# Performance work log

Measured on AMD Instinct MI355X. Metric: run time of the kernel, lower is better.

## Reference

```python
import jax, jax.numpy as jnp
import numpy as np

B, S, L = 4, 1024, 128
H, D = 16, 64            # num_attention_heads, attention_head_size
HID = H * D              # 1024
MAX_POS = 1024


def setup_inputs() -> dict:
    key = jax.random.key(0)
    ks = jax.random.split(key, 12)
    sc = 1.0 / np.sqrt(HID)
    return {
        "hidden_states": jax.random.normal(ks[0], (B, S, HID), jnp.float32),
        "attention_mask": jnp.zeros((B, 1, 1, S), jnp.float32),
        "instruct_hidden_states": jax.random.normal(ks[1], (B, L, HID), jnp.float32),
        "instruct_attention_mask": jnp.zeros((B, 1, 1, L), jnp.float32),
        "Wq": jax.random.normal(ks[2], (HID, HID), jnp.float32) * sc,
        "bq": jnp.zeros((HID,), jnp.float32),
        "Wk": jax.random.normal(ks[3], (HID, HID), jnp.float32) * sc,
        "bk": jnp.zeros((HID,), jnp.float32),
        "Wv": jax.random.normal(ks[4], (HID, HID), jnp.float32) * sc,
        "bv": jnp.zeros((HID,), jnp.float32),
        "gate": jnp.zeros((1, H, 1, 1), jnp.float32),
        "dist_emb": jax.random.normal(ks[5], (2 * MAX_POS - 1, D), jnp.float32) * 0.02,
    }


def _heads(x):
    # [B,T,HID] -> [B,H,T,D]
    b, t, _ = x.shape
    return x.reshape(b, t, H, D).transpose(0, 2, 1, 3)


def reference(hidden_states, attention_mask, instruct_hidden_states,
              instruct_attention_mask, Wq, bq, Wk, bk, Wv, bv, gate, dist_emb):
    inv_sqrt_d = 1.0 / jnp.sqrt(jnp.asarray(D, hidden_states.dtype))

    q = _heads(hidden_states @ Wq + bq)            # [B,H,S,D]
    k = _heads(hidden_states @ Wk + bk)
    v = _heads(hidden_states @ Wv + bv)
    ik = _heads(instruct_hidden_states @ Wk + bk)  # [B,H,L,D]
    iv = _heads(instruct_hidden_states @ Wv + bv)

    scores = jnp.einsum('bhld,bhrd->bhlr', q, k)   # [B,H,S,S]

    # relative_key_query positional scores
    pos = jnp.arange(S)
    dist_idx = pos[:, None] - pos[None, :] + MAX_POS - 1   # [S,S]
    pe = dist_emb[dist_idx]                                # [S,S,D]
    scores = scores + jnp.einsum('bhld,lrd->bhlr', q, pe) \
                    + jnp.einsum('bhrd,lrd->bhlr', k, pe)

    scores = scores * inv_sqrt_d + attention_mask
    probs = jax.nn.softmax(scores, axis=-1)
    ctx = jnp.einsum('bhlr,bhrd->bhld', probs, v)          # [B,H,S,D]

    # gated instruction attention
    iscores = jnp.einsum('bhld,bhrd->bhlr', q, ik) * inv_sqrt_d + instruct_attention_mask
    iprobs = jax.nn.softmax(iscores, axis=-1)
    ictx = jnp.einsum('bhlr,bhrd->bhld', iprobs, iv)
    ctx = ctx + jnp.tanh(gate) * ictx

    # [B,H,S,D] -> [B,S,HID]
    return ctx.transpose(0, 2, 1, 3).reshape(B, S, HID)
```

## Files before the change

kernel.cpp:

```cpp
#include <hip/hip_runtime.h>
#include <cmath>

#define NB 4
#define NH 16
#define SD 64
#define SEQ 1024
#define ILEN 128
#define HIDDIM 1024

#define N_HID (NB*SEQ*HIDDIM)
#define N_INS (NB*ILEN*HIDDIM)
#define N_E_SRC (2047*SD)
#define N_E   (2048*SD)
#define N_W   (HIDDIM*HIDDIM)

typedef short bf8 __attribute__((ext_vector_type(8)));
typedef short bf4 __attribute__((ext_vector_type(4)));
typedef float f4  __attribute__((ext_vector_type(4)));

#define MFMA(a,b,c) __builtin_amdgcn_mfma_f32_16x16x32_bf16(a,b,c,0,0,0)

#define SHIFT 12.0f

__device__ __forceinline__ float bf2f(short s) {
    unsigned u = ((unsigned)(unsigned short)s) << 16;
    return __uint_as_float(u);
}
__device__ __forceinline__ short f2bf(float x) {
    unsigned u = __float_as_uint(x);
    u = (u + 0x7FFFu + ((u >> 16) & 1u)) >> 16;
    return (short)u;
}

__global__ __launch_bounds__(256) void cast_flat(
    const float* __restrict__ hid, const float* __restrict__ ins,
    const float* __restrict__ E, short* __restrict__ ws)
{
    int i = (blockIdx.x * 256 + threadIdx.x) * 4;
    short* dhid = ws;
    short* dins = ws + N_HID;
    short* dE   = ws + N_HID + N_INS;
    if (i < N_HID) {
        float4 v = *(const float4*)&hid[i];
        bf4 o; o[0]=f2bf(v.x); o[1]=f2bf(v.y); o[2]=f2bf(v.z); o[3]=f2bf(v.w);
        *(bf4*)&dhid[i] = o;
    } else if (i < N_HID + N_INS) {
        int j = i - N_HID;
        float4 v = *(const float4*)&ins[j];
        bf4 o; o[0]=f2bf(v.x); o[1]=f2bf(v.y); o[2]=f2bf(v.z); o[3]=f2bf(v.w);
        *(bf4*)&dins[j] = o;
    } else {
        int j = i - N_HID - N_INS;
        if (j < N_E) {
            bf4 o;
            if (j < N_E_SRC) {
                float4 v = *(const float4*)&E[j];
                o[0]=f2bf(v.x); o[1]=f2bf(v.y); o[2]=f2bf(v.z); o[3]=f2bf(v.w);
            } else {
                o[0]=0; o[1]=0; o[2]=0; o[3]=0;
            }
            *(bf4*)&dE[j] = o;
        }
    }
}

__global__ __launch_bounds__(256) void cast_wt(
    const float* __restrict__ Wq, const float* __restrict__ Wk,
    const float* __restrict__ Wv, short* __restrict__ dstbase)
{
    const float* W = (blockIdx.z==0) ? Wq : (blockIdx.z==1) ? Wk : Wv;
    short* dst = dstbase + (size_t)blockIdx.z * N_W;
    const int k0 = blockIdx.y*64, n0 = blockIdx.x*64;
    __shared__ float st[64][65];
    const int tid = threadIdx.x;
    #pragma unroll
    for (int rep=0; rep<4; rep++) {
        int u = tid + rep*256;
        int row = u >> 4, col = (u & 15) * 4;
        float4 v = *(const float4*)&W[(size_t)(k0+row)*HIDDIM + n0 + col];
        st[row][col+0]=v.x; st[row][col+1]=v.y; st[row][col+2]=v.z; st[row][col+3]=v.w;
    }
    __syncthreads();
    #pragma unroll
    for (int rep=0; rep<4; rep++) {
        int u = tid + rep*256;
        int nrow = u >> 4, kc = (u & 15) * 4;
        bf4 o;
        #pragma unroll
        for (int j=0;j<4;j++) o[j] = f2bf(st[kc+j][nrow]);
        *(bf4*)&dst[(size_t)(n0+nrow)*HIDDIM + k0 + kc] = o;
    }
}

__global__ __launch_bounds__(256) void proj_mfma(
    const short* __restrict__ hidb, const short* __restrict__ insb,
    const short* __restrict__ WTall,
    const float* __restrict__ bq, const float* __restrict__ bk, const float* __restrict__ bv,
    short* __restrict__ qo, short* __restrict__ ko, short* __restrict__ vTo,
    short* __restrict__ iko, short* __restrict__ ivTo)
{
    const int z = blockIdx.z;
    const int bx = blockIdx.x, by = blockIdx.y;
    if (z==1 && (bx>=16 || by>=4)) return;
    const short* X = z ? insb : hidb;
    const int T   = z ? ILEN : SEQ;
    const int tsh = z ? 7 : 10;
    const int zoff= z ? 1024 : 0;
    const int m0 = by*128, n0 = bx*128;

    __shared__ short Xs[128*72];
    __shared__ short Ws[128*72];

    const int tid=threadIdx.x, w=tid>>6, lane=tid&63, quad=lane>>4, nl=lane&15;
    const int wr = w>>1, wc = w&1;

    f4 acc[4][4];
    #pragma unroll
    for (int ti=0;ti<4;ti++)
      #pragma unroll
      for (int tj=0;tj<4;tj++) { acc[ti][tj][0]=0.f; acc[ti][tj][1]=0.f; acc[ti][tj][2]=0.f; acc[ti][tj][3]=0.f; }

    for (int k0=0; k0<HIDDIM; k0+=64) {
        __syncthreads();
        #pragma unroll
        for (int rep=0; rep<4; rep++) {
            int u = tid + rep*256;
            int row = u >> 3, ch = u & 7;
            *(uint4*)&Xs[row*72 + ch*8] = *(const uint4*)&X[(size_t)(m0+row)*HIDDIM + k0 + ch*8];
            *(uint4*)&Ws[row*72 + ch*8] = *(const uint4*)&WTall[(size_t)(zoff+n0+row)*HIDDIM + k0 + ch*8];
        }
        __syncthreads();
        bf8 a[4][2], b[4][2];
        #pragma unroll
        for (int ti=0;ti<4;ti++)
          #pragma unroll
          for (int s=0;s<2;s++)
            a[ti][s] = *(const bf8*)&Xs[(64*wr + 16*ti + nl)*72 + s*32 + quad*8];
        #pragma unroll
        for (int tj=0;tj<4;tj++)
          #pragma unroll
          for (int s=0;s<2;s++)
            b[tj][s] = *(const bf8*)&Ws[(64*wc + 16*tj + nl)*72 + s*32 + quad*8];
        #pragma unroll
        for (int ti=0;ti<4;ti++)
          #pragma unroll
          for (int tj=0;tj<4;tj++)
            #pragma unroll
            for (int s=0;s<2;s++)
              acc[ti][tj] = MFMA(a[ti][s], b[tj][s], acc[ti][tj]);
    }

    #pragma unroll
    for (int tj=0;tj<4;tj++) {
        const int n = n0 + 64*wc + 16*tj + nl;
        const int nn = n & 1023;
        const int h = nn >> 6, d = nn & 63;
        float bias; short* outp; int mode;
        if (z==0) {
            if (n < 1024)      { bias = bq[nn]; outp = qo;  mode=0; }
            else if (n < 2048) { bias = bk[nn]; outp = ko;  mode=0; }
            else               { bias = bv[nn]; outp = vTo; mode=1; }
        } else {
            if (n < 1024)      { bias = bk[nn]; outp = iko;  mode=0; }
            else               { bias = bv[nn]; outp = ivTo; mode=1; }
        }
        #pragma unroll
        for (int ti=0;ti<4;ti++) {
            const int mb = m0 + 64*wr + 16*ti + quad*4;
            const int bb = mb >> tsh, tt = mb & (T-1);
            if (mode) {
                bf4 o;
                #pragma unroll
                for (int i=0;i<4;i++) o[i] = f2bf(acc[ti][tj][i] + bias);
                *(bf4*)&outp[((size_t)(bb*NH + h)*SD + d)*T + tt] = o;
            } else {
                #pragma unroll
                for (int i=0;i<4;i++)
                    outp[((size_t)(bb*NH + h)*T + tt + i)*SD + d] = f2bf(acc[ti][tj][i] + bias);
            }
        }
    }
}

__global__ __launch_bounds__(256,2) void attn_mfma(
    const short* __restrict__ qg, const short* __restrict__ kg, const short* __restrict__ vTg,
    const short* __restrict__ ikg, const short* __restrict__ ivTg,
    const float* __restrict__ mask, const float* __restrict__ imask,
    const float* __restrict__ gate, const short* __restrict__ Ebf,
    float* __restrict__ out)
{
    const int l0 = blockIdx.x * 64, h = blockIdx.y, b = blockIdx.z;
    const int tid = threadIdx.x, w = tid>>6, lane = tid&63, quad = lane>>4, nl = lane&15;

    __shared__ short keT[128*68];
    __shared__ short ksh[64*72];
    __shared__ short vts[64*72];
    __shared__ short es [128*72];
    short* ps  = ksh;
    short* psi = es;

    const size_t bh = (size_t)(b*NH + h);
    const short* kbase   = kg   + bh*SEQ*SD;
    const short* vTbase  = vTg  + bh*SD*SEQ;
    const short* ikbase  = ikg  + bh*ILEN*SD;
    const short* ivTbase = ivTg + bh*SD*ILEN;

    bf8 aq[2];
    {
        const short* qrow = qg + (bh*SEQ + l0 + 16*w + nl)*SD;
        #pragma unroll
        for (int s=0;s<2;s++) aq[s] = *(const bf8*)&qrow[s*32 + quad*8];
    }

    f4 o1[4], o2[4];
    float l1[4], l2[4];
    #pragma unroll
    for (int t=0;t<4;t++) {
        o1[t][0]=0.f;o1[t][1]=0.f;o1[t][2]=0.f;o1[t][3]=0.f;
        o2[t][0]=0.f;o2[t][1]=0.f;o2[t][2]=0.f;o2[t][3]=0.f;
        l1[t]=0.f; l2[t]=0.f;
    }

    int srci[4]; bool ci[4];
    #pragma unroll
    for (int i=0;i<4;i++) {
        const int d0 = 4*quad + i - nl;
        srci[i] = (lane & 48) | ((d0 - 1) & 15);
        ci[i]   = (d0 >= 1);
    }

    for (int r0=0; r0<SEQ; r0+=64) {
        const int jb = l0 - r0 + 960;
        __syncthreads();
        #pragma unroll
        for (int rep=0; rep<2; rep++) {
            int u = tid + rep*256;
            int row = u >> 3, ch = u & 7;
            *(uint4*)&ksh[row*72 + ch*8] = *(const uint4*)&kbase[(size_t)(r0+row)*SD + ch*8];
            *(uint4*)&vts[row*72 + ch*8] = *(const uint4*)&vTbase[(size_t)row*SEQ + r0 + ch*8];
        }
        if (r0 == 0) {
            #pragma unroll
            for (int rep=0; rep<4; rep++) {
                int u = tid + rep*256;
                int roff = u >> 3, ch = u & 7;
                int g = jb + roff;
                *(uint4*)&es[(g & 127)*72 + ch*8] = *(const uint4*)&Ebf[(size_t)g*SD + ch*8];
            }
        } else {
            #pragma unroll
            for (int rep=0; rep<2; rep++) {
                int u = tid + rep*256;
                int roff = u >> 3, ch = u & 7;
                int g = jb + roff;
                *(uint4*)&es[(g & 127)*72 + ch*8] = *(const uint4*)&Ebf[(size_t)g*SD + ch*8];
            }
        }
        __syncthreads();

        bf8 ak[2];
        #pragma unroll
        for (int s=0;s<2;s++) ak[s] = *(const bf8*)&ksh[(16*w+nl)*72 + s*32 + quad*8];
        f4 sc[4];
        #pragma unroll
        for (int t=0;t<4;t++) { sc[t][0]=0.f; sc[t][1]=0.f; sc[t][2]=0.f; sc[t][3]=0.f; }
        #pragma unroll
        for (int t=0;t<4;t++)
            #pragma unroll
            for (int s=0;s<2;s++) {
                bf8 bk = *(const bf8*)&ksh[(16*t+nl)*72 + s*32 + quad*8];
                sc[t] = MFMA(aq[s], bk, sc[t]);
            }
        f4 qe[5], ke[5];
        #pragma unroll
        for (int j=0;j<5;j++) {
            qe[j][0]=0.f;qe[j][1]=0.f;qe[j][2]=0.f;qe[j][3]=0.f;
            ke[j][0]=0.f;ke[j][1]=0.f;ke[j][2]=0.f;ke[j][3]=0.f;
        }
        #pragma unroll
        for (int j=0;j<5;j++) {
            const int sq = (jb + 16*(w+j)   + nl) & 127;
            const int sk = (jb + 16*(3-w+j) + nl) & 127;
            #pragma unroll
            for (int s=0;s<2;s++) {
                bf8 beq = *(const bf8*)&es[sq*72 + s*32 + quad*8];
                bf8 bek = *(const bf8*)&es[sk*72 + s*32 + quad*8];
                qe[j] = MFMA(aq[s], beq, qe[j]);
                ke[j] = MFMA(ak[s], bek, ke[j]);
            }
        }
        {
            const int rb = 16*w + 4*quad;
            #pragma unroll
            for (int j=0;j<5;j++) {
                const int c = 16*(3-w+j) + nl;
                bf4 pk;
                #pragma unroll
                for (int i=0;i<4;i++) pk[i] = f2bf(ke[j][i]);
                *(bf4*)&keT[c*68 + rb] = pk;
            }
        }
        float mk[4];
        #pragma unroll
        for (int t=0;t<4;t++) mk[t] = mask[b*SEQ + r0 + 16*t + nl] - SHIFT;
        __syncthreads();

        short pbf[4][4];
        #pragma unroll
        for (int i=0;i<4;i++) {
            const int li = 16*w + 4*quad + i;
            #pragma unroll
            for (int t=0;t<4;t++) {
                float v = ci[i] ? qe[4-t][i] : qe[3-t][i];
                const float qadd = __shfl(v, srci[i]);
                const int ri = 16*t + nl;
                const float kadd = bf2f(keT[(li - ri + 63)*68 + ri]);
                const float sval = (sc[t][i] + qadd + kadd)*0.125f + mk[t];
                const float p = __expf(sval);
                pbf[i][t] = f2bf(p);
                l1[i] += p;
            }
        }
        #pragma unroll
        for (int i=0;i<4;i++) {
            const int li = 16*w + quad*4 + i;
            #pragma unroll
            for (int t=0;t<4;t++) ps[li*72 + 16*t + nl] = pbf[i][t];
        }
        #pragma unroll
        for (int s=0;s<2;s++) {
            bf8 ap = *(const bf8*)&ps[(16*w+nl)*72 + s*32 + quad*8];
            #pragma unroll
            for (int t=0;t<4;t++) {
                bf8 bv = *(const bf8*)&vts[(16*t+nl)*72 + s*32 + quad*8];
                o1[t] = MFMA(ap, bv, o1[t]);
            }
        }
    }

    for (int r0=0; r0<ILEN; r0+=64) {
        __syncthreads();
        #pragma unroll
        for (int rep=0; rep<2; rep++) {
            int u = tid + rep*256;
            int row = u >> 3, ch = u & 7;
            *(uint4*)&ksh[row*72 + ch*8] = *(const uint4*)&ikbase[(size_t)(r0+row)*SD + ch*8];
            *(uint4*)&vts[row*72 + ch*8] = *(const uint4*)&ivTbase[(size_t)row*ILEN + r0 + ch*8];
        }
        __syncthreads();

        f4 sc[4];
        #pragma unroll
        for (int t=0;t<4;t++) { sc[t][0]=0.f; sc[t][1]=0.f; sc[t][2]=0.f; sc[t][3]=0.f; }
        #pragma unroll
        for (int t=0;t<4;t++)
            #pragma unroll
            for (int s=0;s<2;s++) {
                bf8 bk = *(const bf8*)&ksh[(16*t+nl)*72 + s*32 + quad*8];
                sc[t] = MFMA(aq[s], bk, sc[t]);
            }
        short pbf[4][4];
        #pragma unroll
        for (int t=0;t<4;t++) {
            const float mkv = imask[b*ILEN + r0 + 16*t + nl] - SHIFT;
            #pragma unroll
            for (int i=0;i<4;i++) {
                const float p = __expf(sc[t][i]*0.125f + mkv);
                pbf[i][t] = f2bf(p);
                l2[i] += p;
            }
        }
        #pragma unroll
        for (int i=0;i<4;i++) {
            const int li = 16*w + quad*4 + i;
            #pragma unroll
            for (int t=0;t<4;t++) psi[li*72 + 16*t + nl] = pbf[i][t];
        }
        #pragma unroll
        for (int s=0;s<2;s++) {
            bf8 ap = *(const bf8*)&psi[(16*w+nl)*72 + s*32 + quad*8];
            #pragma unroll
            for (int t=0;t<4;t++) {
                bf8 bv = *(const bf8*)&vts[(16*t+nl)*72 + s*32 + quad*8];
                o2[t] = MFMA(ap, bv, o2[t]);
            }
        }
    }

    #pragma unroll
    for (int i=0;i<4;i++) {
        #pragma unroll
        for (int off=1; off<16; off<<=1) {
            l1[i] += __shfl_xor(l1[i], off);
            l2[i] += __shfl_xor(l2[i], off);
        }
    }

    const float tg = tanhf(gate[h]);
    #pragma unroll
    for (int i=0;i<4;i++) {
        const int l = l0 + 16*w + quad*4 + i;
        const float inv1 = 1.0f/l1[i], inv2 = 1.0f/l2[i];
        #pragma unroll
        for (int t=0;t<4;t++) {
            const int d = 16*t + nl;
            out[((size_t)(b*SEQ + l)*NH + h)*SD + d] = o1[t][i]*inv1 + tg*(o2[t][i]*inv2);
        }
    }
}

extern "C" void kernel_launch(void* const* d_in, const int* in_sizes, int n_in,
                              void* d_out, int out_size, void* d_ws, size_t ws_size,
                              hipStream_t stream) {
    const float* hidden  = (const float*)d_in[0];
    const float* mask    = (const float*)d_in[1];
    const float* ihidden = (const float*)d_in[2];
    const float* imask   = (const float*)d_in[3];
    const float* Wq   = (const float*)d_in[4];
    const float* bq   = (const float*)d_in[5];
    const float* Wk   = (const float*)d_in[6];
    const float* bk   = (const float*)d_in[7];
    const float* Wv   = (const float*)d_in[8];
    const float* bv   = (const float*)d_in[9];
    const float* gate = (const float*)d_in[10];
    const float* dist = (const float*)d_in[11];
    float* out = (float*)d_out;

    short* ws = (short*)d_ws;
    const size_t OFF_INS = N_HID;
    const size_t OFF_E   = OFF_INS + N_INS;
    const size_t OFF_WT  = OFF_E + N_E;
    const size_t OFF_Q   = OFF_WT + 3*(size_t)N_W;
    const size_t OFF_K   = OFF_Q + N_HID;
    const size_t OFF_VT  = OFF_K + N_HID;
    const size_t OFF_IK  = OFF_VT + N_HID;
    const size_t OFF_IVT = OFF_IK + N_INS;

    cast_flat<<<4736, 256, 0, stream>>>(hidden, ihidden, dist, ws);
    cast_wt<<<dim3(16,16,3), 256, 0, stream>>>(Wq, Wk, Wv, ws + OFF_WT);
    proj_mfma<<<dim3(24,32,2), 256, 0, stream>>>(
        ws, ws + OFF_INS, ws + OFF_WT,
        bq, bk, bv,
        ws + OFF_Q, ws + OFF_K, ws + OFF_VT, ws + OFF_IK, ws + OFF_IVT);
    attn_mfma<<<dim3(16,16,4), 256, 0, stream>>>(
        ws + OFF_Q, ws + OFF_K, ws + OFF_VT, ws + OFF_IK, ws + OFF_IVT,
        mask, imask, gate, ws + OFF_E, out);
}
```

Baseline: 256.4 us.

## Register-prefetch next tiles in projection GEMM and attention loops

Both the QKV projection GEMM and the attention kernel now load the next K/V/E tiles (plus mask values) into registers while the current tile is being computed, then write them to shared memory at the top of the next iteration. The main attention loop also prefetches the first instruction-attention tiles during its final iteration. The aim is to hide global memory latency behind MFMA work. The cost is extra VGPR pressure, which under launch_bounds(256,2) could cause spills or lower occupancy.

```diff
diff --git a/kernel.cpp b/kernel.cpp
--- a/kernel.cpp
+++ b/kernel.cpp
@@ -113,6 +113,7 @@
 
     const int tid=threadIdx.x, w=tid>>6, lane=tid&63, quad=lane>>4, nl=lane&15;
     const int wr = w>>1, wc = w&1;
+    const int srow = tid >> 3, sch = (tid & 7) * 8;
 
     f4 acc[4][4];
     #pragma unroll
@@ -120,16 +121,32 @@
       #pragma unroll
       for (int tj=0;tj<4;tj++) { acc[ti][tj][0]=0.f; acc[ti][tj][1]=0.f; acc[ti][tj][2]=0.f; acc[ti][tj][3]=0.f; }
 
+    uint4 rx[4], rw[4];
+    #pragma unroll
+    for (int rep=0; rep<4; rep++) {
+        const int row = srow + 32*rep;
+        rx[rep] = *(const uint4*)&X[(size_t)(m0+row)*HIDDIM + sch];
+        rw[rep] = *(const uint4*)&WTall[(size_t)(zoff+n0+row)*HIDDIM + sch];
+    }
+
     for (int k0=0; k0<HIDDIM; k0+=64) {
         __syncthreads();
         #pragma unroll
         for (int rep=0; rep<4; rep++) {
-            int u = tid + rep*256;
-            int row = u >> 3, ch = u & 7;
-            *(uint4*)&Xs[row*72 + ch*8] = *(const uint4*)&X[(size_t)(m0+row)*HIDDIM + k0 + ch*8];
-            *(uint4*)&Ws[row*72 + ch*8] = *(const uint4*)&WTall[(size_t)(zoff+n0+row)*HIDDIM + k0 + ch*8];
-        }
-        __syncthreads();
+            const int row = srow + 32*rep;
+            *(uint4*)&Xs[row*72 + sch] = rx[rep];
+            *(uint4*)&Ws[row*72 + sch] = rw[rep];
+        }
+        __syncthreads();
+        if (k0 + 64 < HIDDIM) {
+            const int k1 = k0 + 64;
+            #pragma unroll
+            for (int rep=0; rep<4; rep++) {
+                const int row = srow + 32*rep;
+                rx[rep] = *(const uint4*)&X[(size_t)(m0+row)*HIDDIM + k1 + sch];
+                rw[rep] = *(const uint4*)&WTall[(size_t)(zoff+n0+row)*HIDDIM + k1 + sch];
+            }
+        }
         bf8 a[4][2], b[4][2];
         #pragma unroll
         for (int ti=0;ti<4;ti++)
@@ -191,6 +208,7 @@
 {
     const int l0 = blockIdx.x * 64, h = blockIdx.y, b = blockIdx.z;
     const int tid = threadIdx.x, w = tid>>6, lane = tid&63, quad = lane>>4, nl = lane&15;
+    const int srow = tid >> 3, sch = (tid & 7) * 8;
 
     __shared__ short keT[128*68];
     __shared__ short ksh[64*72];
@@ -229,32 +247,38 @@
         ci[i]   = (d0 >= 1);
     }
 
+    uint4 rk0, rk1, rv0, rv1, re0, re1, re2, re3;
+    float pmn[4];
+    {
+        const int jb0 = l0 + 960;
+        rk0 = *(const uint4*)&kbase[(size_t)srow*SD + sch];
+        rk1 = *(const uint4*)&kbase[(size_t)(srow+32)*SD + sch];
+        rv0 = *(const uint4*)&vTbase[(size_t)srow*SEQ + sch];
+        rv1 = *(const uint4*)&vTbase[(size_t)(srow+32)*SEQ + sch];
+        re0 = *(const uint4*)&Ebf[(size_t)(jb0+srow)*SD + sch];
+        re1 = *(const uint4*)&Ebf[(size_t)(jb0+srow+32)*SD + sch];
+        re2 = *(const uint4*)&Ebf[(size_t)(jb0+srow+64)*SD + sch];
+        re3 = *(const uint4*)&Ebf[(size_t)(jb0+srow+96)*SD + sch];
+        #pragma unroll
+        for (int t=0;t<4;t++) pmn[t] = mask[b*SEQ + 16*t + nl] - SHIFT;
+    }
+
     for (int r0=0; r0<SEQ; r0+=64) {
         const int jb = l0 - r0 + 960;
-        __syncthreads();
-        #pragma unroll
-        for (int rep=0; rep<2; rep++) {
-            int u = tid + rep*256;
-            int row = u >> 3, ch = u & 7;
-            *(uint4*)&ksh[row*72 + ch*8] = *(const uint4*)&kbase[(size_t)(r0+row)*SD + ch*8];
-            *(uint4*)&vts[row*72 + ch*8] = *(const uint4*)&vTbase[(size_t)row*SEQ + r0 + ch*8];
-        }
+        float pm[4];
+        #pragma unroll
+        for (int t=0;t<4;t++) pm[t] = pmn[t];
+
+        __syncthreads();
+        *(uint4*)&ksh[srow*72 + sch]      = rk0;
+        *(uint4*)&ksh[(srow+32)*72 + sch] = rk1;
+        *(uint4*)&vts[srow*72 + sch]      = rv0;
+        *(uint4*)&vts[(srow+32)*72 + sch] = rv1;
+        *(uint4*)&es[((jb+srow)&127)*72 + sch]    = re0;
+        *(uint4*)&es[((jb+srow+32)&127)*72 + sch] = re1;
         if (r0 == 0) {
-            #pragma unroll
-            for (int rep=0; rep<4; rep++) {
-                int u = tid + rep*256;
-                int roff = u >> 3, ch = u & 7;
-                int g = jb + roff;
-                *(uint4*)&es[(g & 127)*72 + ch*8] = *(const uint4*)&Ebf[(size_t)g*SD + ch*8];
-            }
-        } else {
-            #pragma unroll
-            for (int rep=0; rep<2; rep++) {
-                int u = tid + rep*256;
-                int roff = u >> 3, ch = u & 7;
-                int g = jb + roff;
-                *(uint4*)&es[(g & 127)*72 + ch*8] = *(const uint4*)&Ebf[(size_t)g*SD + ch*8];
-            }
+            *(uint4*)&es[((jb+srow+64)&127)*72 + sch] = re2;
+            *(uint4*)&es[((jb+srow+96)&127)*72 + sch] = re3;
         }
         __syncthreads();
 
@@ -300,10 +324,26 @@
                 *(bf4*)&keT[c*68 + rb] = pk;
             }
         }
-        float mk[4];
-        #pragma unroll
-        for (int t=0;t<4;t++) mk[t] = mask[b*SEQ + r0 + 16*t + nl] - SHIFT;
-        __syncthreads();
+        __syncthreads();
+
+        if (r0 + 64 < SEQ) {
+            const int r1 = r0 + 64, jbn = jb - 64;
+            rk0 = *(const uint4*)&kbase[(size_t)(r1+srow)*SD + sch];
+            rk1 = *(const uint4*)&kbase[(size_t)(r1+srow+32)*SD + sch];
+            rv0 = *(const uint4*)&vTbase[(size_t)srow*SEQ + r1 + sch];
+            rv1 = *(const uint4*)&vTbase[(size_t)(srow+32)*SEQ + r1 + sch];
+            re0 = *(const uint4*)&Ebf[(size_t)(jbn+srow)*SD + sch];
+            re1 = *(const uint4*)&Ebf[(size_t)(jbn+srow+32)*SD + sch];
+            #pragma unroll
+            for (int t=0;t<4;t++) pmn[t] = mask[b*SEQ + r1 + 16*t + nl] - SHIFT;
+        } else {
+            rk0 = *(const uint4*)&ikbase[(size_t)srow*SD + sch];
+            rk1 = *(const uint4*)&ikbase[(size_t)(srow+32)*SD + sch];
+            rv0 = *(const uint4*)&ivTbase[(size_t)srow*ILEN + sch];
+            rv1 = *(const uint4*)&ivTbase[(size_t)(srow+32)*ILEN + sch];
+            #pragma unroll
+            for (int t=0;t<4;t++) pmn[t] = imask[b*ILEN + 16*t + nl] - SHIFT;
+        }
 
         short pbf[4][4];
         #pragma unroll
@@ -315,7 +355,7 @@
                 const float qadd = __shfl(v, srci[i]);
                 const int ri = 16*t + nl;
                 const float kadd = bf2f(keT[(li - ri + 63)*68 + ri]);
-                const float sval = (sc[t][i] + qadd + kadd)*0.125f + mk[t];
+                const float sval = (sc[t][i] + qadd + kadd)*0.125f + pm[t];
                 const float p = __expf(sval);
                 pbf[i][t] = f2bf(p);
                 l1[i] += p;
@@ -339,15 +379,25 @@
     }
 
     for (int r0=0; r0<ILEN; r0+=64) {
-        __syncthreads();
-        #pragma unroll
-        for (int rep=0; rep<2; rep++) {
-            int u = tid + rep*256;
-            int row = u >> 3, ch = u & 7;
-            *(uint4*)&ksh[row*72 + ch*8] = *(const uint4*)&ikbase[(size_t)(r0+row)*SD + ch*8];
-            *(uint4*)&vts[row*72 + ch*8] = *(const uint4*)&ivTbase[(size_t)row*ILEN + r0 + ch*8];
-        }
-        __syncthreads();
+        float im[4];
+        #pragma unroll
+        for (int t=0;t<4;t++) im[t] = pmn[t];
+
+        __syncthreads();
+        *(uint4*)&ksh[srow*72 + sch]      = rk0;
+        *(uint4*)&ksh[(srow+32)*72 + sch] = rk1;
+        *(uint4*)&vts[srow*72 + sch]      = rv0;
+        *(uint4*)&vts[(srow+32)*72 + sch] = rv1;
+        __syncthreads();
+
+        if (r0 == 0) {
+            rk0 = *(const uint4*)&ikbase[(size_t)(64+srow)*SD + sch];
+            rk1 = *(const uint4*)&ikbase[(size_t)(64+srow+32)*SD + sch];
+            rv0 = *(const uint4*)&ivTbase[(size_t)srow*ILEN + 64 + sch];
+            rv1 = *(const uint4*)&ivTbase[(size_t)(srow+32)*ILEN + 64 + sch];
+            #pragma unroll
+            for (int t=0;t<4;t++) pmn[t] = imask[b*ILEN + 64 + 16*t + nl] - SHIFT;
+        }
 
         f4 sc[4];
         #pragma unroll
@@ -362,10 +412,9 @@
         short pbf[4][4];
         #pragma unroll
         for (int t=0;t<4;t++) {
-            const float mkv = imask[b*ILEN + r0 + 16*t + nl] - SHIFT;
             #pragma unroll
             for (int i=0;i<4;i++) {
-                const float p = __expf(sc[t][i]*0.125f + mkv);
+                const float p = __expf(sc[t][i]*0.125f + im[t]);
                 pbf[i][t] = f2bf(p);
                 l2[i] += p;
             }
```

New measurement: 347.2 us. 35.4% more time.

## Double attention query tile to 128 rows per block with shared key-position products

Applied to the files above, without the earlier changes.

The attention kernel now runs 512 threads covering 128 query rows per block, so each K/V tile and relative-position embedding window is loaded once for twice as many queries. The key-times-embedding products are split across the two wave halves (5 and 4 column tiles) and written once to a larger shared keT buffer, which removes duplicated ke MFMA work between neighbouring query tiles. The probability buffer is moved into keT, which needs an extra barrier per tile. Shared memory grows and the grid halves to 512 blocks, which may reduce occupancy and load balance across CUs.

```diff
diff --git a/kernel.cpp b/kernel.cpp
--- a/kernel.cpp
+++ b/kernel.cpp
@@ -182,21 +182,23 @@
     }
 }
 
-__global__ __launch_bounds__(256,2) void attn_mfma(
+__global__ __launch_bounds__(512,4) void attn_mfma(
     const short* __restrict__ qg, const short* __restrict__ kg, const short* __restrict__ vTg,
     const short* __restrict__ ikg, const short* __restrict__ ivTg,
     const float* __restrict__ mask, const float* __restrict__ imask,
     const float* __restrict__ gate, const short* __restrict__ Ebf,
     float* __restrict__ out)
 {
-    const int l0 = blockIdx.x * 64, h = blockIdx.y, b = blockIdx.z;
+    const int l0 = blockIdx.x * 128, h = blockIdx.y, b = blockIdx.z;
     const int tid = threadIdx.x, w = tid>>6, lane = tid&63, quad = lane>>4, nl = lane&15;
-
-    __shared__ short keT[128*68];
+    const int kt = w & 3, half = w >> 2;
+    const int srow = tid >> 3, sch = (tid & 7) * 8;
+
+    __shared__ short keT[192*68];
     __shared__ short ksh[64*72];
     __shared__ short vts[64*72];
-    __shared__ short es [128*72];
-    short* ps  = ksh;
+    __shared__ short es [256*72];
+    short* ps  = keT;
     short* psi = es;
 
     const size_t bh = (size_t)(b*NH + h);
@@ -229,38 +231,60 @@
         ci[i]   = (d0 >= 1);
     }
 
+    const int nj  = half ? 4 : 5;
+    const int ct0 = (half ? 8 : 3) - kt;
+
     for (int r0=0; r0<SEQ; r0+=64) {
         const int jb = l0 - r0 + 960;
         __syncthreads();
-        #pragma unroll
-        for (int rep=0; rep<2; rep++) {
-            int u = tid + rep*256;
-            int row = u >> 3, ch = u & 7;
-            *(uint4*)&ksh[row*72 + ch*8] = *(const uint4*)&kbase[(size_t)(r0+row)*SD + ch*8];
-            *(uint4*)&vts[row*72 + ch*8] = *(const uint4*)&vTbase[(size_t)row*SEQ + r0 + ch*8];
-        }
+        *(uint4*)&ksh[srow*72 + sch] = *(const uint4*)&kbase[(size_t)(r0+srow)*SD + sch];
+        *(uint4*)&vts[srow*72 + sch] = *(const uint4*)&vTbase[(size_t)srow*SEQ + r0 + sch];
         if (r0 == 0) {
             #pragma unroll
-            for (int rep=0; rep<4; rep++) {
-                int u = tid + rep*256;
-                int roff = u >> 3, ch = u & 7;
-                int g = jb + roff;
-                *(uint4*)&es[(g & 127)*72 + ch*8] = *(const uint4*)&Ebf[(size_t)g*SD + ch*8];
+            for (int p=0; p<3; p++) {
+                const int g = jb + 64*p + srow;
+                *(uint4*)&es[(g & 255)*72 + sch] = *(const uint4*)&Ebf[(size_t)g*SD + sch];
             }
         } else {
-            #pragma unroll
-            for (int rep=0; rep<2; rep++) {
-                int u = tid + rep*256;
-                int roff = u >> 3, ch = u & 7;
-                int g = jb + roff;
-                *(uint4*)&es[(g & 127)*72 + ch*8] = *(const uint4*)&Ebf[(size_t)g*SD + ch*8];
-            }
-        }
-        __syncthreads();
+            const int g = jb + srow;
+            *(uint4*)&es[(g & 255)*72 + sch] = *(const uint4*)&Ebf[(size_t)g*SD + sch];
+        }
+        __syncthreads();
+
+        float mk[4];
+        #pragma unroll
+        for (int t=0;t<4;t++) mk[t] = mask[b*SEQ + r0 + 16*t + nl] - SHIFT;
 
         bf8 ak[2];
         #pragma unroll
-        for (int s=0;s<2;s++) ak[s] = *(const bf8*)&ksh[(16*w+nl)*72 + s*32 + quad*8];
+        for (int s=0;s<2;s++) ak[s] = *(const bf8*)&ksh[(16*kt+nl)*72 + s*32 + quad*8];
+        {
+            f4 ke[5];
+            #pragma unroll
+            for (int j=0;j<5;j++) { ke[j][0]=0.f;ke[j][1]=0.f;ke[j][2]=0.f;ke[j][3]=0.f; }
+            #pragma unroll
+            for (int j=0;j<5;j++) {
+                if (j < nj) {
+                    const int slot = (jb + 16*(ct0+j) + nl) & 255;
+                    #pragma unroll
+                    for (int s=0;s<2;s++) {
+                        bf8 bek = *(const bf8*)&es[slot*72 + s*32 + quad*8];
+                        ke[j] = MFMA(ak[s], bek, ke[j]);
+                    }
+                }
+            }
+            const int rb = 16*kt + 4*quad;
+            #pragma unroll
+            for (int j=0;j<5;j++) {
+                if (j < nj) {
+                    const int c = 16*(ct0+j) + nl;
+                    bf4 pk;
+                    #pragma unroll
+                    for (int i=0;i<4;i++) pk[i] = f2bf(ke[j][i]);
+                    *(bf4*)&keT[c*68 + rb] = pk;
+                }
+            }
+        }
         f4 sc[4];
         #pragma unroll
         for (int t=0;t<4;t++) { sc[t][0]=0.f; sc[t][1]=0.f; sc[t][2]=0.f; sc[t][3]=0.f; }
@@ -271,38 +295,18 @@
                 bf8 bk = *(const bf8*)&ksh[(16*t+nl)*72 + s*32 + quad*8];
                 sc[t] = MFMA(aq[s], bk, sc[t]);
             }
-        f4 qe[5], ke[5];
+        f4 qe[5];
+        #pragma unroll
+        for (int j=0;j<5;j++) { qe[j][0]=0.f;qe[j][1]=0.f;qe[j][2]=0.f;qe[j][3]=0.f; }
         #pragma unroll
         for (int j=0;j<5;j++) {
-            qe[j][0]=0.f;qe[j][1]=0.f;qe[j][2]=0.f;qe[j][3]=0.f;
-            ke[j][0]=0.f;ke[j][1]=0.f;ke[j][2]=0.f;ke[j][3]=0.f;
-        }
-        #pragma unroll
-        for (int j=0;j<5;j++) {
-            const int sq = (jb + 16*(w+j)   + nl) & 127;
-            const int sk = (jb + 16*(3-w+j) + nl) & 127;
+            const int slot = (jb + 16*(w+j) + nl) & 255;
             #pragma unroll
             for (int s=0;s<2;s++) {
-                bf8 beq = *(const bf8*)&es[sq*72 + s*32 + quad*8];
-                bf8 bek = *(const bf8*)&es[sk*72 + s*32 + quad*8];
+                bf8 beq = *(const bf8*)&es[slot*72 + s*32 + quad*8];
                 qe[j] = MFMA(aq[s], beq, qe[j]);
-                ke[j] = MFMA(ak[s], bek, ke[j]);
-            }
-        }
-        {
-            const int rb = 16*w + 4*quad;
-            #pragma unroll
-            for (int j=0;j<5;j++) {
-                const int c = 16*(3-w+j) + nl;
-                bf4 pk;
-                #pragma unroll
-                for (int i=0;i<4;i++) pk[i] = f2bf(ke[j][i]);
-                *(bf4*)&keT[c*68 + rb] = pk;
-            }
-        }
-        float mk[4];
-        #pragma unroll
-        for (int t=0;t<4;t++) mk[t] = mask[b*SEQ + r0 + 16*t + nl] - SHIFT;
+            }
+        }
         __syncthreads();
 
         short pbf[4][4];
@@ -321,6 +325,8 @@
                 l1[i] += p;
             }
         }
+        __syncthreads();
+
         #pragma unroll
         for (int i=0;i<4;i++) {
             const int li = 16*w + quad*4 + i;
@@ -340,14 +346,13 @@
 
     for (int r0=0; r0<ILEN; r0+=64) {
         __syncthreads();
-        #pragma unroll
-        for (int rep=0; rep<2; rep++) {
-            int u = tid + rep*256;
-            int row = u >> 3, ch = u & 7;
-            *(uint4*)&ksh[row*72 + ch*8] = *(const uint4*)&ikbase[(size_t)(r0+row)*SD + ch*8];
-            *(uint4*)&vts[row*72 + ch*8] = *(const uint4*)&ivTbase[(size_t)row*ILEN + r0 + ch*8];
-        }
-        __syncthreads();
+        *(uint4*)&ksh[srow*72 + sch] = *(const uint4*)&ikbase[(size_t)(r0+srow)*SD + sch];
+        *(uint4*)&vts[srow*72 + sch] = *(const uint4*)&ivTbase[(size_t)srow*ILEN + r0 + sch];
+        __syncthreads();
+
+        float im[4];
+        #pragma unroll
+        for (int t=0;t<4;t++) im[t] = imask[b*ILEN + r0 + 16*t + nl] - SHIFT;
 
         f4 sc[4];
         #pragma unroll
@@ -362,10 +367,9 @@
         short pbf[4][4];
         #pragma unroll
         for (int t=0;t<4;t++) {
-            const float mkv = imask[b*ILEN + r0 + 16*t + nl] - SHIFT;
             #pragma unroll
             for (int i=0;i<4;i++) {
-                const float p = __expf(sc[t][i]*0.125f + mkv);
+                const float p = __expf(sc[t][i]*0.125f + im[t]);
                 pbf[i][t] = f2bf(p);
                 l2[i] += p;
             }
@@ -442,7 +446,7 @@
         ws, ws + OFF_INS, ws + OFF_WT,
         bq, bk, bv,
         ws + OFF_Q, ws + OFF_K, ws + OFF_VT, ws + OFF_IK, ws + OFF_IVT);
-    attn_mfma<<<dim3(16,16,4), 256, 0, stream>>>(
+    attn_mfma<<<dim3(8,16,4), 512, 0, stream>>>(
         ws + OFF_Q, ws + OFF_K, ws + OFF_VT, ws + OFF_IK, ws + OFF_IVT,
         mask, imask, gate, ws + OFF_E, out);
 }
```

New measurement: 239.7 us. -6.5%, faster.
